# Kernel optimization log

Hardware: AMD Instinct MI355X
Metric: run time of the kernel (lower is better)

Reference implementation:

```python
import jax, jax.numpy as jnp
import numpy as np

H = 8
DK = 64          # d_model // h
D_MODEL = 512
DIM_G = 64       # trignometric geometry embedding dim
WAVE_LEN = 1000.0


def box_relational_embedding(boxes):
    # boxes: [B, N, 4] = (x_min, y_min, x_max, y_max)
    x_min, y_min, x_max, y_max = [boxes[..., i:i + 1] for i in range(4)]  # each [B,N,1]
    cx = (x_min + x_max) * 0.5
    cy = (y_min + y_max) * 0.5
    w = (x_max - x_min) + 1.0
    h = (y_max - y_min) + 1.0

    def rel(c, s):
        # log(clamp(|c_i - c_j| / s_i, 1e-3)) -> [B,N,N]
        return jnp.log(jnp.clip(jnp.abs((c - jnp.swapaxes(c, -2, -1)) / s), 1e-3, None))

    delta_x = rel(cx, w)
    delta_y = rel(cy, h)
    delta_w = jnp.log(w / jnp.swapaxes(w, -2, -1))
    delta_h = jnp.log(h / jnp.swapaxes(h, -2, -1))
    pos = jnp.stack([delta_x, delta_y, delta_w, delta_h], axis=-1)  # [B,N,N,4]

    n_freq = DIM_G // 8  # 8 frequencies per geometric feature
    feat_range = jnp.arange(n_freq, dtype=pos.dtype)
    dim_mat = 1.0 / (WAVE_LEN ** (feat_range / n_freq))            # [n_freq]
    mul = (100.0 * pos)[..., None] * dim_mat                        # [B,N,N,4,n_freq]
    B, N = pos.shape[0], pos.shape[1]
    mul = mul.reshape(B, N, N, 4 * n_freq)                          # [B,N,N,32]
    return jnp.concatenate([jnp.sin(mul), jnp.cos(mul)], axis=-1)   # [B,N,N,64]


def setup_inputs() -> dict:
    key = jax.random.key(0)
    ks = jax.random.split(key, 14)
    B, N = 4, 512
    s = 0.02
    return {
        "input_query": jax.random.normal(ks[0], (B, N, D_MODEL), jnp.float32),
        "input_key":   jax.random.normal(ks[1], (B, N, D_MODEL), jnp.float32),
        "input_value": jax.random.normal(ks[2], (B, N, D_MODEL), jnp.float32),
        "input_box":   jax.random.uniform(ks[3], (B, N, 4), jnp.float32),
        "Wq": jax.random.normal(ks[4], (D_MODEL, D_MODEL), jnp.float32) * s,
        "bq": jax.random.normal(ks[5], (D_MODEL,), jnp.float32) * s,
        "Wk": jax.random.normal(ks[6], (D_MODEL, D_MODEL), jnp.float32) * s,
        "bk": jax.random.normal(ks[7], (D_MODEL,), jnp.float32) * s,
        "Wv": jax.random.normal(ks[8], (D_MODEL, D_MODEL), jnp.float32) * s,
        "bv": jax.random.normal(ks[9], (D_MODEL,), jnp.float32) * s,
        "Wo": jax.random.normal(ks[10], (D_MODEL, D_MODEL), jnp.float32) * s,
        "bo": jax.random.normal(ks[11], (D_MODEL,), jnp.float32) * s,
        "WG": jax.random.normal(ks[12], (H, DIM_G), jnp.float32) * s,
        "bG": jax.random.normal(ks[13], (H,), jnp.float32) * s,
    }


def reference(input_query, input_key, input_value, input_box,
              Wq, bq, Wk, bk, Wv, bv, Wo, bo, WG, bG):
    B, N, _ = input_query.shape

    # geometry log-bias per head: relu(Linear_h(emb)) -> [B,H,N,N]
    emb = box_relational_embedding(input_box)                        # [B,N,N,64]
    wg = jax.nn.relu(jnp.einsum('bmng,hg->bhmn', emb, WG)
                     + bG[None, :, None, None])

    def proj(x, W, b):
        # torch Linear: x @ W^T + b, then split heads -> [B,H,N,DK]
        y = x @ W.T + b
        return y.reshape(B, N, H, DK).transpose(0, 2, 1, 3)

    q = proj(input_query, Wq, bq)
    k = proj(input_key, Wk, bk)
    v = proj(input_value, Wv, bv)

    scale = 1.0 / jnp.sqrt(jnp.asarray(DK, q.dtype))
    scores = jnp.einsum('bhqd,bhkd->bhqk', q, k) * scale             # [B,H,N,N]
    logits = jnp.log(jnp.clip(wg, 1e-6, None)) + scores
    attn = jax.nn.softmax(logits, axis=-1)                           # dropout is identity in eval
    out = jnp.einsum('bhqk,bhkd->bhqd', attn, v)
    out = out.transpose(0, 2, 1, 3).reshape(B, N, H * DK)
    return out @ Wo.T + bo
```

## Files before the change

### kernel.cpp

```cpp
#include <hip/hip_runtime.h>
#include <hip/hip_bf16.h>
#include <cstdint>

typedef unsigned short u16;
typedef unsigned int u32;
typedef __attribute__((ext_vector_type(8))) short short8;
typedef __attribute__((ext_vector_type(4))) float f32x4;
typedef __attribute__((ext_vector_type(4))) unsigned int u32x4;
typedef __attribute__((ext_vector_type(4))) unsigned short u16x4;

#define REV 15.91549431f

__device__ __forceinline__ u16 f2b(float x) { return __builtin_bit_cast(u16, (__bf16)x); }
__device__ __forceinline__ u16 f2h(float x) { return __builtin_bit_cast(u16, (_Float16)x); }
__device__ __forceinline__ float c_dim_f(int f) {
    const float c[8] = {1.0f, 0.42169650f, 0.17782794f, 0.074989421f,
                        0.031622777f, 0.013335214f, 0.0056234132f, 0.0023713737f};
    return c[f];
}
__device__ __forceinline__ void gload_lds16(const void* g, void* l) {
    __builtin_amdgcn_global_load_lds((const __attribute__((address_space(1))) u32*)g,
                                     (__attribute__((address_space(3))) u32*)l, 16, 0, 0);
}

__global__ __launch_bounds__(256) void prep_k(const float* __restrict__ s0,
                                              const float* __restrict__ s1,
                                              const float* __restrict__ s2,
                                              const float* __restrict__ s3,
                                              const float* __restrict__ s4,
                                              const float* __restrict__ s5,
                                              const float* __restrict__ s6,
                                              const float* __restrict__ box,
                                              const float* __restrict__ WG,
                                              const float* __restrict__ bG,
                                              u16* __restrict__ dstX,
                                              u16* __restrict__ dstW,
                                              u16* __restrict__ outW) {
    __shared__ char embs[256 * 128];
    const int z = blockIdx.z;
    const int t = threadIdx.x;

    if (z < 7) {
        const float* s;
        u16* dst;
        if (z < 3) {
            s = (z == 0) ? s0 : (z == 1) ? s1 : s2;
            dst = dstX + (size_t)z * 1048576;
        } else {
            if (blockIdx.x >= 256) return;
            s = (z == 3) ? s3 : (z == 4) ? s4 : (z == 5) ? s5 : s6;
            dst = dstW + (size_t)(z - 3) * 262144;
        }
        int i = (blockIdx.x * 256 + t) * 4;
        float4 v = *(const float4*)&s[i];
        u16x4 o = { f2b(v.x), f2b(v.y), f2b(v.z), f2b(v.w) };
        *(u16x4*)&dst[i] = o;
        return;
    }

    const int wave = t >> 6, lane = t & 63;
    const int b = z - 7;
    const int jt = blockIdx.x & 1, ii = blockIdx.x >> 1;
    const int j = (jt << 8) + t;
    const int swz = (t & 7) << 4;

    float4 bi = *(const float4*)&box[(size_t)(((b << 9) + ii) << 2)];
    float4 bj = *(const float4*)&box[(size_t)(((b << 9) + j) << 2)];
    float cxi = (bi.x + bi.z) * 0.5f, cyi = (bi.y + bi.w) * 0.5f;
    float wdi = bi.z - bi.x + 1.0f,   hgi = bi.w - bi.y + 1.0f;
    float cxj = (bj.x + bj.z) * 0.5f, cyj = (bj.y + bj.w) * 0.5f;
    float wdj = bj.z - bj.x + 1.0f,   hgj = bj.w - bj.y + 1.0f;

    float pos[4];
    pos[0] = __logf(fmaxf(fabsf((cxi - cxj) / wdi), 1e-3f));
    pos[1] = __logf(fmaxf(fabsf((cyi - cyj) / hgi), 1e-3f));
    pos[2] = __logf(wdi) - __logf(wdj);
    pos[3] = __logf(hgi) - __logf(hgj);

#pragma unroll
    for (int p = 0; p < 4; p++) {
        float rev = pos[p] * REV;
        u32x4 sp, cp;
#pragma unroll
        for (int f = 0; f < 4; f++) {
            float a0 = rev * c_dim_f(2 * f), a1 = rev * c_dim_f(2 * f + 1);
            sp[f] = (u32)f2b(__builtin_amdgcn_sinf(a0)) | ((u32)f2b(__builtin_amdgcn_sinf(a1)) << 16);
            cp[f] = (u32)f2b(__builtin_amdgcn_cosf(a0)) | ((u32)f2b(__builtin_amdgcn_cosf(a1)) << 16);
        }
        *(u32x4*)(embs + (((t << 7) + (p << 4)) ^ swz)) = sp;
        *(u32x4*)(embs + (((t << 7) + 64 + (p << 4)) ^ swz)) = cp;
    }

    const int hh = lane & 15;
    const int ko = (lane >> 4) << 3;
    short8 bf0 = {0,0,0,0,0,0,0,0}, bf1 = {0,0,0,0,0,0,0,0};
    float bGh = 0.0f;
    if (hh < 8) {
        const float* wrow = WG + hh * 64;
#pragma unroll
        for (int e = 0; e < 8; e++) {
            bf0[e] = (short)f2b(wrow[ko + e]);
            bf1[e] = (short)f2b(wrow[32 + ko + e]);
        }
        bGh = bG[hh];
    }
    __syncthreads();

#pragma unroll
    for (int tt = 0; tt < 4; tt++) {
        int mt = (wave << 2) + tt;
        int row = (mt << 4) + hh;
        int rswz = (row & 7) << 4;
        short8 a0v = *(const short8*)(embs + (((row << 7) + (ko << 1)) ^ rswz));
        short8 a1v = *(const short8*)(embs + (((row << 7) + 64 + (ko << 1)) ^ rswz));
        f32x4 acc = {0.f, 0.f, 0.f, 0.f};
        acc = __builtin_amdgcn_mfma_f32_16x16x32_bf16(a0v, bf0, acc, 0, 0, 0);
        acc = __builtin_amdgcn_mfma_f32_16x16x32_bf16(a1v, bf1, acc, 0, 0, 0);
        if (hh < 8) {
            int j0 = (jt << 8) + (mt << 4) + ((lane >> 4) << 2);
            u16x4 ow;
#pragma unroll
            for (int r = 0; r < 4; r++)
                ow[r] = f2h(fmaxf(acc[r] + bGh, 1e-6f) * 1024.0f);
            *(u16x4*)&outW[((size_t)((b << 3) + hh) << 18) + ((size_t)ii << 9) + j0] = ow;
        }
    }
}

__global__ __launch_bounds__(256) void attn_k(const u16* __restrict__ Qb,
                                              const u16* __restrict__ Kb,
                                              const u16* __restrict__ VT,
                                              const u16* __restrict__ Wp,
                                              u16* __restrict__ ATT) {
    __shared__ u16 Pl[4][16 * 68];
    __shared__ float Mrg[3][64][25];
    const int t = threadIdx.x;
    const int wave = t >> 6, lane = t & 63;
    const int c = lane & 15, g = lane >> 4;
    const int bid = blockIdx.x;
    const int qb = bid & 31, bh = bid >> 5;
    const int b = bh >> 3, h = bh & 7;
    const int q0 = qb << 4;

    const u16* Qp = Qb + ((size_t)bh << 15);
    const u16* Kp = Kb + ((size_t)bh << 15);
    const u16* Vp = VT + ((size_t)bh << 15);
    const _Float16* Bp = (const _Float16*)Wp + ((size_t)bh << 18) + ((size_t)q0 << 9);

    short8 qf[2];
#pragma unroll
    for (int ks = 0; ks < 2; ks++)
        qf[ks] = *(const short8*)&Qp[(size_t)(q0 + c) * 64 + ks * 32 + g * 8];

    f32x4 o[4] = {};
    float m[4] = {-1e30f, -1e30f, -1e30f, -1e30f};
    float l[4] = {0.f, 0.f, 0.f, 0.f};

    for (int kt = 0; kt < 2; kt++) {
        const int k0 = ((wave << 1) + kt) << 6;
        short8 kf[4][2], vf[4][2];
#pragma unroll
        for (int jj = 0; jj < 4; jj++)
#pragma unroll
            for (int ks = 0; ks < 2; ks++) {
                kf[jj][ks] = *(const short8*)&Kp[(size_t)(k0 + jj * 16 + c) * 64 + ks * 32 + g * 8];
                vf[jj][ks] = *(const short8*)&Vp[(size_t)(jj * 16 + c) * 512 + k0 + ks * 32 + g * 8];
            }
        float wgt[4][4];
#pragma unroll
        for (int jj = 0; jj < 4; jj++)
#pragma unroll
            for (int r = 0; r < 4; r++)
                wgt[jj][r] = (float)Bp[(size_t)(g * 4 + r) * 512 + k0 + jj * 16 + c];

        f32x4 sa[4] = {};
        __builtin_amdgcn_s_setprio(1);
#pragma unroll
        for (int jj = 0; jj < 4; jj++)
#pragma unroll
            for (int ks = 0; ks < 2; ks++)
                sa[jj] = __builtin_amdgcn_mfma_f32_16x16x32_bf16(qf[ks], kf[jj][ks], sa[jj], 0, 0, 0);
        __builtin_amdgcn_s_setprio(0);

        float s[4][4];
#pragma unroll
        for (int r = 0; r < 4; r++) {
#pragma unroll
            for (int jj = 0; jj < 4; jj++)
                s[jj][r] = sa[jj][r] * 0.125f;
            float v = fmaxf(fmaxf(s[0][r], s[1][r]), fmaxf(s[2][r], s[3][r]));
#pragma unroll
            for (int off = 1; off < 16; off <<= 1)
                v = fmaxf(v, __shfl_xor(v, off));
            float mn = fmaxf(m[r], v);
            float alpha = __expf(m[r] - mn);
            m[r] = mn;
            float rs = 0.f;
#pragma unroll
            for (int jj = 0; jj < 4; jj++) {
                float p = wgt[jj][r] * __expf(s[jj][r] - mn);
                s[jj][r] = p;
                rs += p;
            }
#pragma unroll
            for (int off = 1; off < 16; off <<= 1)
                rs += __shfl_xor(rs, off);
            l[r] = l[r] * alpha + rs;
#pragma unroll
            for (int jjo = 0; jjo < 4; jjo++)
                o[jjo][r] *= alpha;
        }

#pragma unroll
        for (int jj = 0; jj < 4; jj++)
#pragma unroll
            for (int r = 0; r < 4; r++)
                Pl[wave][(g * 4 + r) * 68 + jj * 16 + c] = f2b(s[jj][r]);
        asm volatile("s_waitcnt lgkmcnt(0)" ::: "memory");
        __builtin_amdgcn_sched_barrier(0);

        short8 pa[2];
#pragma unroll
        for (int ks = 0; ks < 2; ks++)
            pa[ks] = *(const short8*)&Pl[wave][c * 68 + ks * 32 + g * 8];
        __builtin_amdgcn_s_setprio(1);
#pragma unroll
        for (int jjo = 0; jjo < 4; jjo++)
#pragma unroll
            for (int ks = 0; ks < 2; ks++)
                o[jjo] = __builtin_amdgcn_mfma_f32_16x16x32_bf16(pa[ks], vf[jjo][ks], o[jjo], 0, 0, 0);
        __builtin_amdgcn_s_setprio(0);
        __builtin_amdgcn_sched_barrier(0);
    }

    if (wave > 0) {
#pragma unroll
        for (int r = 0; r < 4; r++) {
            Mrg[wave - 1][lane][r] = m[r];
            Mrg[wave - 1][lane][4 + r] = l[r];
#pragma unroll
            for (int jjo = 0; jjo < 4; jjo++)
                Mrg[wave - 1][lane][8 + jjo * 4 + r] = o[jjo][r];
        }
    }
    __syncthreads();
    if (wave == 0) {
#pragma unroll
        for (int w = 0; w < 3; w++) {
#pragma unroll
            for (int r = 0; r < 4; r++) {
                float m1 = Mrg[w][lane][r];
                float l1 = Mrg[w][lane][4 + r];
                float mn = fmaxf(m[r], m1);
                float a0 = __expf(m[r] - mn), a1 = __expf(m1 - mn);
                m[r] = mn;
                l[r] = l[r] * a0 + l1 * a1;
#pragma unroll
                for (int jjo = 0; jjo < 4; jjo++)
                    o[jjo][r] = o[jjo][r] * a0 + Mrg[w][lane][8 + jjo * 4 + r] * a1;
            }
        }
#pragma unroll
        for (int r = 0; r < 4; r++) {
            float inv = 1.0f / l[r];
            int row = q0 + g * 4 + r;
#pragma unroll
            for (int jjo = 0; jjo < 4; jjo++)
                ATT[(size_t)(((b << 9) + row) << 9) + (h << 6) + jjo * 16 + c] = f2b(o[jjo][r] * inv);
        }
    }
}

__global__ __launch_bounds__(256) void proj_k(const u16* __restrict__ Xall,
                                              const u16* __restrict__ Wall,
                                              const float* __restrict__ bq,
                                              const float* __restrict__ bk,
                                              const float* __restrict__ bv,
                                              u16* __restrict__ Qb,
                                              u16* __restrict__ Kb,
                                              u16* __restrict__ VT) {
    __shared__ u16 As[64 * 32];
    __shared__ u16 Bs[64 * 32];

    const int t = threadIdx.x;
    const int wave = t >> 6, lane = t & 63;
    const int wr = wave >> 1, wc = wave & 1;
    const int m0 = blockIdx.y * 64, n0 = blockIdx.x * 64;
    const int z = blockIdx.z;

    const u16* A  = Xall + (size_t)z * 1048576;
    const u16* Bm = Wall + (size_t)z * 262144;
    const float* bias = (z == 0) ? bq : (z == 1) ? bk : bv;
    u16* out = (z == 0) ? Qb : (z == 1) ? Kb : VT;

    f32x4 acc[2][2] = {};
    const int srow = t >> 2;
    const int scol = (((t & 3) ^ ((t >> 3) & 3)) << 3);
    const int c = lane & 15, g = lane >> 4;
    const int gsw = (g ^ ((c >> 1) & 3)) << 3;

    for (int k0 = 0; k0 < 512; k0 += 32) {
        gload_lds16(&A[(size_t)(m0 + srow) * 512 + k0 + scol], &As[t * 8]);
        gload_lds16(&Bm[(size_t)(n0 + srow) * 512 + k0 + scol], &Bs[t * 8]);
        __syncthreads();
        short8 af[2], bfr[2];
#pragma unroll
        for (int i = 0; i < 2; i++)
            af[i] = *(const short8*)&As[(wr * 32 + i * 16 + c) * 32 + gsw];
#pragma unroll
        for (int jj = 0; jj < 2; jj++)
            bfr[jj] = *(const short8*)&Bs[(wc * 32 + jj * 16 + c) * 32 + gsw];
#pragma unroll
        for (int i = 0; i < 2; i++)
#pragma unroll
            for (int jj = 0; jj < 2; jj++)
                acc[i][jj] = __builtin_amdgcn_mfma_f32_16x16x32_bf16(af[i], bfr[jj], acc[i][jj], 0, 0, 0);
        __syncthreads();
    }

#pragma unroll
    for (int i = 0; i < 2; i++)
#pragma unroll
        for (int jj = 0; jj < 2; jj++)
#pragma unroll
            for (int r = 0; r < 4; r++) {
                int row = m0 + wr * 32 + i * 16 + ((lane >> 4) << 2) + r;
                int col = n0 + wc * 32 + jj * 16 + (lane & 15);
                float v = acc[i][jj][r] + bias[col];
                int b = row >> 9, rr = row & 511, h = col >> 6, d = col & 63;
                if (z < 2)
                    out[(size_t)((((b << 3) + h) << 9) + rr) * 64 + d] = f2b(v);
                else
                    out[(size_t)((((b << 3) + h) << 6) + d) * 512 + rr] = f2b(v);
            }
}

__global__ __launch_bounds__(256) void outg_k(const u16* __restrict__ A,
                                              const u16* __restrict__ Bm,
                                              const float* __restrict__ bias,
                                              float* __restrict__ outF) {
    __shared__ u16 As[64 * 32];
    __shared__ u16 Bs[64 * 32];

    const int t = threadIdx.x;
    const int wave = t >> 6, lane = t & 63;
    const int wr = wave >> 1, wc = wave & 1;
    const int m0 = blockIdx.y * 64, n0 = blockIdx.x * 64;

    f32x4 acc[2][2] = {};
    const int srow = t >> 2;
    const int scol = (((t & 3) ^ ((t >> 3) & 3)) << 3);
    const int c = lane & 15, g = lane >> 4;
    const int gsw = (g ^ ((c >> 1) & 3)) << 3;

    for (int k0 = 0; k0 < 512; k0 += 32) {
        gload_lds16(&A[(size_t)(m0 + srow) * 512 + k0 + scol], &As[t * 8]);
        gload_lds16(&Bm[(size_t)(n0 + srow) * 512 + k0 + scol], &Bs[t * 8]);
        __syncthreads();
        short8 af[2], bfr[2];
#pragma unroll
        for (int i = 0; i < 2; i++)
            af[i] = *(const short8*)&As[(wr * 32 + i * 16 + c) * 32 + gsw];
#pragma unroll
        for (int jj = 0; jj < 2; jj++)
            bfr[jj] = *(const short8*)&Bs[(wc * 32 + jj * 16 + c) * 32 + gsw];
#pragma unroll
        for (int i = 0; i < 2; i++)
#pragma unroll
            for (int jj = 0; jj < 2; jj++)
                acc[i][jj] = __builtin_amdgcn_mfma_f32_16x16x32_bf16(af[i], bfr[jj], acc[i][jj], 0, 0, 0);
        __syncthreads();
    }

#pragma unroll
    for (int i = 0; i < 2; i++)
#pragma unroll
        for (int jj = 0; jj < 2; jj++)
#pragma unroll
            for (int r = 0; r < 4; r++) {
                int row = m0 + wr * 32 + i * 16 + ((lane >> 4) << 2) + r;
                int col = n0 + wc * 32 + jj * 16 + (lane & 15);
                outF[((size_t)row << 9) + col] = acc[i][jj][r] + bias[col];
            }
}

extern "C" void kernel_launch(void* const* d_in, const int* in_sizes, int n_in,
                              void* d_out, int out_size, void* d_ws, size_t ws_size,
                              hipStream_t stream) {
    const float* inq = (const float*)d_in[0];
    const float* ink = (const float*)d_in[1];
    const float* inv = (const float*)d_in[2];
    const float* box = (const float*)d_in[3];
    const float* Wq  = (const float*)d_in[4];
    const float* bq  = (const float*)d_in[5];
    const float* Wk  = (const float*)d_in[6];
    const float* bk  = (const float*)d_in[7];
    const float* Wv  = (const float*)d_in[8];
    const float* bv  = (const float*)d_in[9];
    const float* Wo  = (const float*)d_in[10];
    const float* bo  = (const float*)d_in[11];
    const float* WG  = (const float*)d_in[12];
    const float* bG  = (const float*)d_in[13];

    u16* base = (u16*)d_ws;
    u16* Xall = base;
    u16* Wall = base + 3145728;
    u16* Qb   = base + 4194304;
    u16* Kb   = base + 5242880;
    u16* VT   = base + 6291456;
    u16* ATT  = base + 7340032;
    u16* Wp   = base + 8388608;

    prep_k<<<dim3(1024, 1, 11), 256, 0, stream>>>(inq, ink, inv, Wq, Wk, Wv, Wo,
                                                  box, WG, bG, Xall, Wall, Wp);

    proj_k<<<dim3(8, 32, 3), 256, 0, stream>>>(Xall, Wall, bq, bk, bv, Qb, Kb, VT);

    attn_k<<<dim3(1024), 256, 0, stream>>>(Qb, Kb, VT, Wp, ATT);

    outg_k<<<dim3(8, 32, 1), 256, 0, stream>>>(ATT, Wall + 786432, bo, (float*)d_out);
}
```

Measured before the change: 70.41 us.

## Double-buffer LDS tiles in projection and output GEMM kernels

Both the QKV projection and output projection GEMMs now use two LDS buffers. The next K-slice is prefetched via global_load_lds while MFMAs run on the current one, with explicit vmcnt waits and raw s_barrier in place of __syncthreads. This is meant to hide global-to-LDS load latency in the main loop. It doubles LDS use per block and depends on the hand-written waitcnt counts being correct.

```diff
diff --git a/kernel.cpp b/kernel.cpp
--- a/kernel.cpp
+++ b/kernel.cpp
@@ -279,8 +279,8 @@
                                               u16* __restrict__ Qb,
                                               u16* __restrict__ Kb,
                                               u16* __restrict__ VT) {
-    __shared__ u16 As[64 * 32];
-    __shared__ u16 Bs[64 * 32];
+    __shared__ u16 As[2][64 * 32];
+    __shared__ u16 Bs[2][64 * 32];
 
     const int t = threadIdx.x;
     const int wave = t >> 6, lane = t & 63;
@@ -299,23 +299,37 @@
     const int c = lane & 15, g = lane >> 4;
     const int gsw = (g ^ ((c >> 1) & 3)) << 3;
 
-    for (int k0 = 0; k0 < 512; k0 += 32) {
-        gload_lds16(&A[(size_t)(m0 + srow) * 512 + k0 + scol], &As[t * 8]);
-        gload_lds16(&Bm[(size_t)(n0 + srow) * 512 + k0 + scol], &Bs[t * 8]);
-        __syncthreads();
+    const size_t arow = (size_t)(m0 + srow) * 512 + scol;
+    const size_t brow = (size_t)(n0 + srow) * 512 + scol;
+
+    gload_lds16(&A[arow], &As[0][t * 8]);
+    gload_lds16(&Bm[brow], &Bs[0][t * 8]);
+
+    int cur = 0;
+    for (int k0 = 0; k0 < 512; k0 += 32, cur ^= 1) {
+        if (k0 + 32 < 512) {
+            gload_lds16(&A[arow + k0 + 32], &As[cur ^ 1][t * 8]);
+            gload_lds16(&Bm[brow + k0 + 32], &Bs[cur ^ 1][t * 8]);
+            asm volatile("s_waitcnt vmcnt(2)" ::: "memory");
+        } else {
+            asm volatile("s_waitcnt vmcnt(0)" ::: "memory");
+        }
+        __builtin_amdgcn_s_barrier();
+        __builtin_amdgcn_sched_barrier(0);
         short8 af[2], bfr[2];
 #pragma unroll
         for (int i = 0; i < 2; i++)
-            af[i] = *(const short8*)&As[(wr * 32 + i * 16 + c) * 32 + gsw];
+            af[i] = *(const short8*)&As[cur][(wr * 32 + i * 16 + c) * 32 + gsw];
 #pragma unroll
         for (int jj = 0; jj < 2; jj++)
-            bfr[jj] = *(const short8*)&Bs[(wc * 32 + jj * 16 + c) * 32 + gsw];
+            bfr[jj] = *(const short8*)&Bs[cur][(wc * 32 + jj * 16 + c) * 32 + gsw];
 #pragma unroll
         for (int i = 0; i < 2; i++)
 #pragma unroll
             for (int jj = 0; jj < 2; jj++)
                 acc[i][jj] = __builtin_amdgcn_mfma_f32_16x16x32_bf16(af[i], bfr[jj], acc[i][jj], 0, 0, 0);
-        __syncthreads();
+        __builtin_amdgcn_sched_barrier(0);
+        __builtin_amdgcn_s_barrier();
     }
 
 #pragma unroll
@@ -339,8 +353,8 @@
                                               const u16* __restrict__ Bm,
                                               const float* __restrict__ bias,
                                               float* __restrict__ outF) {
-    __shared__ u16 As[64 * 32];
-    __shared__ u16 Bs[64 * 32];
+    __shared__ u16 As[2][64 * 32];
+    __shared__ u16 Bs[2][64 * 32];
 
     const int t = threadIdx.x;
     const int wave = t >> 6, lane = t & 63;
@@ -353,23 +367,37 @@
     const int c = lane & 15, g = lane >> 4;
     const int gsw = (g ^ ((c >> 1) & 3)) << 3;
 
-    for (int k0 = 0; k0 < 512; k0 += 32) {
-        gload_lds16(&A[(size_t)(m0 + srow) * 512 + k0 + scol], &As[t * 8]);
-        gload_lds16(&Bm[(size_t)(n0 + srow) * 512 + k0 + scol], &Bs[t * 8]);
-        __syncthreads();
+    const size_t arow = (size_t)(m0 + srow) * 512 + scol;
+    const size_t brow = (size_t)(n0 + srow) * 512 + scol;
+
+    gload_lds16(&A[arow], &As[0][t * 8]);
+    gload_lds16(&Bm[brow], &Bs[0][t * 8]);
+
+    int cur = 0;
+    for (int k0 = 0; k0 < 512; k0 += 32, cur ^= 1) {
+        if (k0 + 32 < 512) {
+            gload_lds16(&A[arow + k0 + 32], &As[cur ^ 1][t * 8]);
+            gload_lds16(&Bm[brow + k0 + 32], &Bs[cur ^ 1][t * 8]);
+            asm volatile("s_waitcnt vmcnt(2)" ::: "memory");
+        } else {
+            asm volatile("s_waitcnt vmcnt(0)" ::: "memory");
+        }
+        __builtin_amdgcn_s_barrier();
+        __builtin_amdgcn_sched_barrier(0);
         short8 af[2], bfr[2];
 #pragma unroll
         for (int i = 0; i < 2; i++)
-            af[i] = *(const short8*)&As[(wr * 32 + i * 16 + c) * 32 + gsw];
+            af[i] = *(const short8*)&As[cur][(wr * 32 + i * 16 + c) * 32 + gsw];
 #pragma unroll
         for (int jj = 0; jj < 2; jj++)
-            bfr[jj] = *(const short8*)&Bs[(wc * 32 + jj * 16 + c) * 32 + gsw];
+            bfr[jj] = *(const short8*)&Bs[cur][(wc * 32 + jj * 16 + c) * 32 + gsw];
 #pragma unroll
         for (int i = 0; i < 2; i++)
 #pragma unroll
             for (int jj = 0; jj < 2; jj++)
                 acc[i][jj] = __builtin_amdgcn_mfma_f32_16x16x32_bf16(af[i], bfr[jj], acc[i][jj], 0, 0, 0);
-        __syncthreads();
+        __builtin_amdgcn_sched_barrier(0);
+        __builtin_amdgcn_s_barrier();
     }
 
 #pragma unroll
```

Result: no change. 70.37 us (-0.1%).
